# Kernel tuning notes

Hardware: AMD Instinct MI355X
Metric: run time of the kernel (lower is better)

## Reference

```python
import jax, jax.numpy as jnp
import numpy as np
import math

HIDDEN = 768
KEY = 128      # attention_key_size
INTER = 1536   # intermediate_size
B, S = 4, 2048


def setup_inputs() -> dict:
    key = jax.random.key(0)
    ks = jax.random.split(key, 8)
    hidden_states = jax.random.normal(ks[0], (B, S, HIDDEN), dtype=jnp.float32)
    attention_mask = jax.random.randint(ks[1], (B, 1, 1, S), 0, 2, dtype=jnp.int32)
    position_ids = jnp.arange(B * S, dtype=jnp.int32).reshape(B, S) % S
    Wi = jax.random.normal(ks[2], (HIDDEN, 2 * INTER + KEY), dtype=jnp.float32) * 0.02
    bi = jnp.zeros((2 * INTER + KEY,), dtype=jnp.float32)
    gamma = jax.random.normal(ks[3], (2, KEY), dtype=jnp.float32) * 0.02 + 1.0
    beta = jnp.zeros((2, KEY), dtype=jnp.float32)
    Wo = jax.random.normal(ks[4], (INTER, HIDDEN), dtype=jnp.float32) * 0.02
    bo = jnp.zeros((HIDDEN,), dtype=jnp.float32)
    return {"hidden_states": hidden_states, "attention_mask": attention_mask,
            "position_ids": position_ids, "Wi": Wi, "bi": bi,
            "gamma": gamma, "beta": beta, "Wo": Wo, "bo": bo}


def _gau_forward(hidden_states, attention_mask, Wi, bi, gamma, beta, Wo, bo):
    # i_dense + swish activation
    h = jax.nn.silu(jnp.einsum('bsd,de->bse', hidden_states, Wi) + bi)
    u = h[..., :INTER]
    v = h[..., INTER:2 * INTER]
    qk = h[..., 2 * INTER:]
    # OffsetScale: per-head affine (heads=2 -> q, k)
    q = qk * gamma[0] + beta[0]
    k = qk * gamma[1] + beta[1]
    scores = jnp.einsum('bid,bjd->bij', q, k) / math.sqrt(KEY)
    # additive mask: (1 - m) * -1e12, squeeze head dim
    am = (1.0 - attention_mask.astype(scores.dtype)) * -1e12
    scores = scores + am[:, 0]  # [B,1,S] broadcasts over query dim
    # softmax_plus normalization: scale logits by log(l)/log(512)
    valid = (scores > -1e11).astype(scores.dtype)
    l = jnp.maximum(jnp.sum(valid, axis=-1, keepdims=True), 1.0)
    scale = jnp.log(l) / jnp.log(jnp.asarray(512.0, scores.dtype))
    attn = jax.nn.softmax(scores * scale, axis=-1)
    ctx = jnp.einsum('bij,bjd->bid', attn, v)
    return jnp.einsum('bse,eh->bsh', u * ctx, Wo) + bo


def reference(hidden_states, attention_mask, position_ids, Wi, bi, gamma, beta, Wo, bo):
    # position_ids unused: p_bias is not 'rotary'
    return _gau_forward(hidden_states, attention_mask, Wi, bi, gamma, beta, Wo, bo)
```

## Files before the change

### kernel.cpp

```cpp
#include <hip/hip_runtime.h>
#include <math.h>

#define HIDDEN 768
#define KEY    128
#define INTER  1536
#define NB     4
#define SEQ    2048
#define MTOT   (NB*SEQ)
#define ETOT   (2*INTER+KEY)

typedef short bf16x8 __attribute__((ext_vector_type(8)));
typedef float f32x4  __attribute__((ext_vector_type(4)));

__device__ __forceinline__ unsigned short f2bfbits(float x) {
    union { float f; unsigned int u; } a; a.f = x;
    unsigned int r = a.u + 0x7fffu + ((a.u >> 16) & 1u);
    return (unsigned short)(r >> 16);
}
__device__ __forceinline__ float bfbits2f(unsigned short b) {
    union { float f; unsigned int u; } a; a.u = ((unsigned int)b) << 16;
    return a.f;
}

__device__ __forceinline__ void gl2lds16(const unsigned short* g, unsigned short* l) {
    __builtin_amdgcn_global_load_lds(
        (const __attribute__((address_space(1))) unsigned int*)g,
        (__attribute__((address_space(3))) unsigned int*)l, 16, 0, 0);
}

__global__ __launch_bounds__(256) void scale_kernel(const int* __restrict__ mask,
                                                    float* __restrict__ scaleb) {
    __shared__ int red[256];
    int b = blockIdx.x;
    int s = 0;
    for (int j = threadIdx.x; j < SEQ; j += 256)
        s += (mask[b*SEQ + j] != 0) ? 1 : 0;
    red[threadIdx.x] = s;
    __syncthreads();
    for (int step = 128; step > 0; step >>= 1) {
        if (threadIdx.x < step) red[threadIdx.x] += red[threadIdx.x + step];
        __syncthreads();
    }
    if (threadIdx.x == 0) {
        float l = fmaxf((float)red[0], 1.0f);
        scaleb[b] = logf(l) / logf(512.0f);
    }
}

__global__ __launch_bounds__(256) void cvt_bf16_kernel(const float* __restrict__ in,
                                                       unsigned short* __restrict__ out, int n4) {
    int i = blockIdx.x*256 + threadIdx.x;
    if (i < n4) {
        float4 v = ((const float4*)in)[i];
        ushort4 o;
        o.x = f2bfbits(v.x); o.y = f2bfbits(v.y);
        o.z = f2bfbits(v.z); o.w = f2bfbits(v.w);
        ((ushort4*)out)[i] = o;
    }
}

__global__ __launch_bounds__(256) void transpose_cvt(const float* __restrict__ in,
                                                     unsigned short* __restrict__ out,
                                                     int R, int C) {
    __shared__ unsigned short tile[32][33];
    int c0 = blockIdx.x*32, r0 = blockIdx.y*32;
    int tx = threadIdx.x & 31, ty4 = (threadIdx.x >> 5)*4;
    #pragma unroll
    for (int rr = 0; rr < 4; rr++) {
        int r = ty4 + rr;
        tile[r][tx] = f2bfbits(in[(size_t)(r0+r)*C + c0+tx]);
    }
    __syncthreads();
    #pragma unroll
    for (int rr = 0; rr < 4; rr++) {
        int r = ty4 + rr;
        out[(size_t)(c0+r)*R + r0+tx] = tile[tx][r];
    }
}

__global__ __launch_bounds__(256) void transpose_v(const unsigned short* __restrict__ v,
                                                   unsigned short* __restrict__ vT) {
    __shared__ unsigned short tile[32][33];
    int z = blockIdx.z;
    int c0 = blockIdx.x*32, s0 = blockIdx.y*32;
    int tx = threadIdx.x & 31, ty4 = (threadIdx.x >> 5)*4;
    #pragma unroll
    for (int rr = 0; rr < 4; rr++) {
        int s = ty4 + rr;
        tile[s][tx] = v[(size_t)(z*SEQ + s0+s)*INTER + c0+tx];
    }
    __syncthreads();
    #pragma unroll
    for (int rr = 0; rr < 4; rr++) {
        int c = ty4 + rr;
        vT[((size_t)z*INTER + c0+c)*SEQ + s0+tx] = tile[tx][c];
    }
}

__device__ __forceinline__ void mfma_core(
    const unsigned short* __restrict__ Abase, int lda,
    const unsigned short* __restrict__ Bbase, int ldb,
    unsigned short* As, unsigned short* Bs,
    f32x4 acc[4][4], int tid, int ktot)
{
    const int lane = tid & 63, wave = tid >> 6;
    const int wm = (wave >> 1) << 6, wn = (wave & 1) << 6;
    const int lm = lane & 15;
    const int q8 = (lane >> 4) << 3;
    const int row_a = tid >> 2, col_a = (tid & 3) << 3;
    const int row_b = row_a + 64;

    for (int k0 = 0; k0 < ktot; k0 += 32) {
        if (k0) __syncthreads();
        gl2lds16(Abase + (size_t)row_a*lda + k0 + col_a, As + tid*8);
        gl2lds16(Bbase + (size_t)row_a*ldb + k0 + col_a, Bs + tid*8);
        gl2lds16(Abase + (size_t)row_b*lda + k0 + col_a, As + (tid+256)*8);
        gl2lds16(Bbase + (size_t)row_b*ldb + k0 + col_a, Bs + (tid+256)*8);
        __syncthreads();
        bf16x8 af[4], bfr[4];
        #pragma unroll
        for (int i = 0; i < 4; i++)
            af[i] = *(const bf16x8*)&As[(wm + i*16 + lm)*32 + q8];
        #pragma unroll
        for (int j = 0; j < 4; j++)
            bfr[j] = *(const bf16x8*)&Bs[(wn + j*16 + lm)*32 + q8];
        #pragma unroll
        for (int i = 0; i < 4; i++)
            #pragma unroll
            for (int j = 0; j < 4; j++)
                acc[i][j] = __builtin_amdgcn_mfma_f32_16x16x32_bf16(af[i], bfr[j], acc[i][j], 0, 0, 0);
    }
}

#define EPILOG_IDX \
    const int lane = tid & 63, wave = tid >> 6; \
    const int wm = (wave >> 1) << 6, wn = (wave & 1) << 6; \
    const int cn = lane & 15, r4 = (lane >> 4) << 2;

__global__ __launch_bounds__(256) void gemm1_mfma(
    const unsigned short* __restrict__ Xb, const unsigned short* __restrict__ WiT,
    const float* __restrict__ bi, const float* __restrict__ gamma, const float* __restrict__ beta,
    unsigned short* __restrict__ u, unsigned short* __restrict__ v,
    unsigned short* __restrict__ qb, unsigned short* __restrict__ kb)
{
    __shared__ __align__(16) unsigned short As[128*32];
    __shared__ __align__(16) unsigned short Bs[128*32];
    const int tid = threadIdx.x;
    const int row0 = blockIdx.y*128, col0 = blockIdx.x*128;
    f32x4 acc[4][4];
    #pragma unroll
    for (int i = 0; i < 4; i++)
        #pragma unroll
        for (int j = 0; j < 4; j++)
            acc[i][j] = (f32x4){0.f,0.f,0.f,0.f};
    mfma_core(Xb + (size_t)row0*HIDDEN, HIDDEN, WiT + (size_t)col0*HIDDEN, HIDDEN,
              As, Bs, acc, tid, HIDDEN);
    EPILOG_IDX
    #pragma unroll
    for (int j = 0; j < 4; j++) {
        int n = col0 + wn + j*16 + cn;
        float bin = bi[n];
        #pragma unroll
        for (int i = 0; i < 4; i++) {
            #pragma unroll
            for (int r = 0; r < 4; r++) {
                int m = row0 + wm + i*16 + r4 + r;
                float x = acc[i][j][r] + bin;
                float h = x / (1.0f + __expf(-x));
                if (col0 < INTER) {
                    u[(size_t)m*INTER + n] = f2bfbits(h);
                } else if (col0 < 2*INTER) {
                    v[(size_t)m*INTER + (n - INTER)] = f2bfbits(h);
                } else {
                    int c = n - 2*INTER;
                    qb[(size_t)m*KEY + c] = f2bfbits(h*gamma[c]       + beta[c]);
                    kb[(size_t)m*KEY + c] = f2bfbits(h*gamma[KEY + c] + beta[KEY + c]);
                }
            }
        }
    }
}

__global__ __launch_bounds__(256) void attn_mfma(
    const unsigned short* __restrict__ qb, const unsigned short* __restrict__ kb,
    const int* __restrict__ mask, const float* __restrict__ scaleb,
    unsigned short* __restrict__ P)
{
    __shared__ __align__(16) unsigned short As[128*32];
    __shared__ __align__(16) unsigned short Bs[128*32];
    const int tid = threadIdx.x;
    const int z = blockIdx.z;
    const int row0 = blockIdx.y*128, col0 = blockIdx.x*128;
    f32x4 acc[4][4];
    #pragma unroll
    for (int i = 0; i < 4; i++)
        #pragma unroll
        for (int j = 0; j < 4; j++)
            acc[i][j] = (f32x4){0.f,0.f,0.f,0.f};
    mfma_core(qb + ((size_t)z*SEQ + row0)*KEY, KEY, kb + ((size_t)z*SEQ + col0)*KEY, KEY,
              As, Bs, acc, tid, KEY);
    const float st = scaleb[z] * 0.08838834764831845f;
    EPILOG_IDX
    #pragma unroll
    for (int j = 0; j < 4; j++) {
        int n = col0 + wn + j*16 + cn;
        int mk = mask[z*SEQ + n];
        #pragma unroll
        for (int i = 0; i < 4; i++) {
            #pragma unroll
            for (int r = 0; r < 4; r++) {
                int m = row0 + wm + i*16 + r4 + r;
                float p = mk ? __expf(acc[i][j][r]*st) : 0.0f;
                P[((size_t)z*SEQ + m)*SEQ + n] = f2bfbits(p);
            }
        }
    }
}

__global__ __launch_bounds__(256) void rowsum_kernel(const unsigned short* __restrict__ P,
                                                     float* __restrict__ lbuf) {
    int row = blockIdx.x*4 + (threadIdx.x >> 6);
    int lane = threadIdx.x & 63;
    const unsigned short* pr = P + (size_t)row*SEQ;
    float s = 0.f;
    for (int c = lane*8; c < SEQ; c += 64*8) {
        ushort4 a = *(const ushort4*)&pr[c];
        ushort4 b = *(const ushort4*)&pr[c+4];
        s += bfbits2f(a.x)+bfbits2f(a.y)+bfbits2f(a.z)+bfbits2f(a.w)
           + bfbits2f(b.x)+bfbits2f(b.y)+bfbits2f(b.z)+bfbits2f(b.w);
    }
    #pragma unroll
    for (int off = 32; off > 0; off >>= 1) s += __shfl_down(s, off, 64);
    if (lane == 0) lbuf[row] = s;
}

__global__ __launch_bounds__(256) void pv_mfma(
    const unsigned short* __restrict__ P, const unsigned short* __restrict__ vT,
    const float* __restrict__ lbuf, unsigned short* __restrict__ u)
{
    __shared__ __align__(16) unsigned short As[128*32];
    __shared__ __align__(16) unsigned short Bs[128*32];
    const int tid = threadIdx.x;
    const int z = blockIdx.z;
    const int row0 = blockIdx.y*128, col0 = blockIdx.x*128;
    f32x4 acc[4][4];
    #pragma unroll
    for (int i = 0; i < 4; i++)
        #pragma unroll
        for (int j = 0; j < 4; j++)
            acc[i][j] = (f32x4){0.f,0.f,0.f,0.f};
    mfma_core(P + ((size_t)z*SEQ + row0)*SEQ, SEQ, vT + ((size_t)z*INTER + col0)*SEQ, SEQ,
              As, Bs, acc, tid, SEQ);
    EPILOG_IDX
    #pragma unroll
    for (int i = 0; i < 4; i++) {
        #pragma unroll
        for (int r = 0; r < 4; r++) {
            int gm = z*SEQ + row0 + wm + i*16 + r4 + r;
            float linv = 1.0f / lbuf[gm];
            #pragma unroll
            for (int j = 0; j < 4; j++) {
                int n = col0 + wn + j*16 + cn;
                size_t idx = (size_t)gm*INTER + n;
                float uu = bfbits2f(u[idx]);
                u[idx] = f2bfbits(uu * acc[i][j][r] * linv);
            }
        }
    }
}

__global__ __launch_bounds__(256) void gemm2_mfma(
    const unsigned short* __restrict__ g, const unsigned short* __restrict__ WoT,
    const float* __restrict__ bo, float* __restrict__ out)
{
    __shared__ __align__(16) unsigned short As[128*32];
    __shared__ __align__(16) unsigned short Bs[128*32];
    const int tid = threadIdx.x;
    const int row0 = blockIdx.y*128, col0 = blockIdx.x*128;
    f32x4 acc[4][4];
    #pragma unroll
    for (int i = 0; i < 4; i++)
        #pragma unroll
        for (int j = 0; j < 4; j++)
            acc[i][j] = (f32x4){0.f,0.f,0.f,0.f};
    mfma_core(g + (size_t)row0*INTER, INTER, WoT + (size_t)col0*INTER, INTER,
              As, Bs, acc, tid, INTER);
    EPILOG_IDX
    #pragma unroll
    for (int j = 0; j < 4; j++) {
        int n = col0 + wn + j*16 + cn;
        float bon = bo[n];
        #pragma unroll
        for (int i = 0; i < 4; i++) {
            #pragma unroll
            for (int r = 0; r < 4; r++) {
                int m = row0 + wm + i*16 + r4 + r;
                out[(size_t)m*HIDDEN + n] = acc[i][j][r] + bon;
            }
        }
    }
}

extern "C" void kernel_launch(void* const* d_in, const int* in_sizes, int n_in,
                              void* d_out, int out_size, void* d_ws, size_t ws_size,
                              hipStream_t stream)
{
    const float* X     = (const float*)d_in[0];
    const int*   mask  = (const int*)d_in[1];
    const float* Wi    = (const float*)d_in[3];
    const float* bi    = (const float*)d_in[4];
    const float* gamma = (const float*)d_in[5];
    const float* beta  = (const float*)d_in[6];
    const float* Wo    = (const float*)d_in[7];
    const float* bo    = (const float*)d_in[8];
    float* out = (float*)d_out;

    unsigned short* Xb  = (unsigned short*)d_ws;
    unsigned short* WiT = Xb  + (size_t)MTOT*HIDDEN;
    unsigned short* WoT = WiT + (size_t)ETOT*HIDDEN;
    unsigned short* u   = WoT + (size_t)HIDDEN*INTER;
    unsigned short* v   = u   + (size_t)MTOT*INTER;
    unsigned short* vT  = v   + (size_t)MTOT*INTER;
    unsigned short* qb  = vT  + (size_t)MTOT*INTER;
    unsigned short* kb  = qb  + (size_t)MTOT*KEY;
    unsigned short* P   = kb  + (size_t)MTOT*KEY;
    float* lb  = (float*)(P + (size_t)NB*SEQ*SEQ);
    float* scb = lb + MTOT;

    scale_kernel<<<NB, 256, 0, stream>>>(mask, scb);
    cvt_bf16_kernel<<<(MTOT*HIDDEN/4 + 255)/256, 256, 0, stream>>>(X, Xb, MTOT*HIDDEN/4);
    transpose_cvt<<<dim3(ETOT/32, HIDDEN/32), 256, 0, stream>>>(Wi, WiT, HIDDEN, ETOT);
    transpose_cvt<<<dim3(HIDDEN/32, INTER/32), 256, 0, stream>>>(Wo, WoT, INTER, HIDDEN);
    gemm1_mfma<<<dim3(ETOT/128, MTOT/128), 256, 0, stream>>>(Xb, WiT, bi, gamma, beta, u, v, qb, kb);
    transpose_v<<<dim3(INTER/32, SEQ/32, NB), 256, 0, stream>>>(v, vT);
    attn_mfma<<<dim3(SEQ/128, SEQ/128, NB), 256, 0, stream>>>(qb, kb, mask, scb, P);
    rowsum_kernel<<<MTOT/4, 256, 0, stream>>>(P, lb);
    pv_mfma<<<dim3(INTER/128, SEQ/128, NB), 256, 0, stream>>>(P, vT, lb, u);
    gemm2_mfma<<<dim3(HIDDEN/128, MTOT/128), 256, 0, stream>>>(u, WoT, bo, out);
}
```

Before: 328.5 us.

## Stage GEMM epilogues through LDS for vectorized stores and fuse V transpose

The epilogues of gemm1, attn and pv now write their accumulator tiles into a padded shared-memory buffer, then emit 16-byte vectorized global stores instead of scattered 2-byte stores. gemm1 writes V directly in transposed layout from LDS, so the separate transpose_v kernel and the v buffer are gone. The pv epilogue now rounds the context to bf16 before multiplying by u, which adds a small extra rounding step. Shared memory per block grows to 128x136 shorts, which may reduce occupancy, and the extra barriers add some sync cost.

```diff
diff --git a/kernel.cpp b/kernel.cpp
--- a/kernel.cpp
+++ b/kernel.cpp
@@ -8,9 +8,11 @@
 #define SEQ    2048
 #define MTOT   (NB*SEQ)
 #define ETOT   (2*INTER+KEY)
+#define CS     136
 
 typedef short bf16x8 __attribute__((ext_vector_type(8)));
 typedef float f32x4  __attribute__((ext_vector_type(4)));
+typedef unsigned short u16x8 __attribute__((ext_vector_type(8)));
 
 __device__ __forceinline__ unsigned short f2bfbits(float x) {
     union { float f; unsigned int u; } a; a.f = x;
@@ -78,25 +80,6 @@
     }
 }
 
-__global__ __launch_bounds__(256) void transpose_v(const unsigned short* __restrict__ v,
-                                                   unsigned short* __restrict__ vT) {
-    __shared__ unsigned short tile[32][33];
-    int z = blockIdx.z;
-    int c0 = blockIdx.x*32, s0 = blockIdx.y*32;
-    int tx = threadIdx.x & 31, ty4 = (threadIdx.x >> 5)*4;
-    #pragma unroll
-    for (int rr = 0; rr < 4; rr++) {
-        int s = ty4 + rr;
-        tile[s][tx] = v[(size_t)(z*SEQ + s0+s)*INTER + c0+tx];
-    }
-    __syncthreads();
-    #pragma unroll
-    for (int rr = 0; rr < 4; rr++) {
-        int c = ty4 + rr;
-        vT[((size_t)z*INTER + c0+c)*SEQ + s0+tx] = tile[tx][c];
-    }
-}
-
 __device__ __forceinline__ void mfma_core(
     const unsigned short* __restrict__ Abase, int lda,
     const unsigned short* __restrict__ Bbase, int ldb,
@@ -140,11 +123,12 @@
 __global__ __launch_bounds__(256) void gemm1_mfma(
     const unsigned short* __restrict__ Xb, const unsigned short* __restrict__ WiT,
     const float* __restrict__ bi, const float* __restrict__ gamma, const float* __restrict__ beta,
-    unsigned short* __restrict__ u, unsigned short* __restrict__ v,
+    unsigned short* __restrict__ u, unsigned short* __restrict__ vT,
     unsigned short* __restrict__ qb, unsigned short* __restrict__ kb)
 {
-    __shared__ __align__(16) unsigned short As[128*32];
-    __shared__ __align__(16) unsigned short Bs[128*32];
+    __shared__ __align__(16) unsigned short smem[128*CS];
+    unsigned short* As = smem;
+    unsigned short* Bs = smem + 4096;
     const int tid = threadIdx.x;
     const int row0 = blockIdx.y*128, col0 = blockIdx.x*128;
     f32x4 acc[4][4];
@@ -156,27 +140,61 @@
     mfma_core(Xb + (size_t)row0*HIDDEN, HIDDEN, WiT + (size_t)col0*HIDDEN, HIDDEN,
               As, Bs, acc, tid, HIDDEN);
     EPILOG_IDX
+    __syncthreads();
     #pragma unroll
     for (int j = 0; j < 4; j++) {
-        int n = col0 + wn + j*16 + cn;
-        float bin = bi[n];
+        int nl = wn + j*16 + cn;
+        float bin = bi[col0 + nl];
         #pragma unroll
         for (int i = 0; i < 4; i++) {
             #pragma unroll
             for (int r = 0; r < 4; r++) {
-                int m = row0 + wm + i*16 + r4 + r;
+                int rowl = wm + i*16 + r4 + r;
                 float x = acc[i][j][r] + bin;
                 float h = x / (1.0f + __expf(-x));
-                if (col0 < INTER) {
-                    u[(size_t)m*INTER + n] = f2bfbits(h);
-                } else if (col0 < 2*INTER) {
-                    v[(size_t)m*INTER + (n - INTER)] = f2bfbits(h);
-                } else {
-                    int c = n - 2*INTER;
-                    qb[(size_t)m*KEY + c] = f2bfbits(h*gamma[c]       + beta[c]);
-                    kb[(size_t)m*KEY + c] = f2bfbits(h*gamma[KEY + c] + beta[KEY + c]);
-                }
-            }
+                smem[rowl*CS + nl] = f2bfbits(h);
+            }
+        }
+    }
+    __syncthreads();
+    if (col0 < INTER) {
+        #pragma unroll
+        for (int rnd = 0; rnd < 8; rnd++) {
+            int row = rnd*16 + (tid>>4);
+            int col = (tid&15)*8;
+            u16x8 h = *(const u16x8*)&smem[row*CS + col];
+            *(u16x8*)&u[(size_t)(row0+row)*INTER + col0 + col] = h;
+        }
+    } else if (col0 < 2*INTER) {
+        int c = tid >> 1;
+        int half = tid & 1;
+        int b = row0 / SEQ;
+        int srow = row0 - b*SEQ + half*64;
+        size_t base = ((size_t)b*INTER + (col0 - INTER) + c)*SEQ + srow;
+        #pragma unroll
+        for (int k = 0; k < 8; k++) {
+            u16x8 h;
+            #pragma unroll
+            for (int t = 0; t < 8; t++)
+                h[t] = smem[(half*64 + k*8 + t)*CS + c];
+            *(u16x8*)&vT[base + k*8] = h;
+        }
+    } else {
+        #pragma unroll
+        for (int rnd = 0; rnd < 8; rnd++) {
+            int row = rnd*16 + (tid>>4);
+            int col = (tid&15)*8;
+            u16x8 h = *(const u16x8*)&smem[row*CS + col];
+            int m = row0 + row;
+            u16x8 qo, ko;
+            #pragma unroll
+            for (int t = 0; t < 8; t++) {
+                float hv = bfbits2f(h[t]);
+                qo[t] = f2bfbits(hv*gamma[col+t]       + beta[col+t]);
+                ko[t] = f2bfbits(hv*gamma[KEY+col+t]   + beta[KEY+col+t]);
+            }
+            *(u16x8*)&qb[(size_t)m*KEY + col] = qo;
+            *(u16x8*)&kb[(size_t)m*KEY + col] = ko;
         }
     }
 }
@@ -186,8 +204,9 @@
     const int* __restrict__ mask, const float* __restrict__ scaleb,
     unsigned short* __restrict__ P)
 {
-    __shared__ __align__(16) unsigned short As[128*32];
-    __shared__ __align__(16) unsigned short Bs[128*32];
+    __shared__ __align__(16) unsigned short smem[128*CS];
+    unsigned short* As = smem;
+    unsigned short* Bs = smem + 4096;
     const int tid = threadIdx.x;
     const int z = blockIdx.z;
     const int row0 = blockIdx.y*128, col0 = blockIdx.x*128;
@@ -201,19 +220,28 @@
               As, Bs, acc, tid, KEY);
     const float st = scaleb[z] * 0.08838834764831845f;
     EPILOG_IDX
+    __syncthreads();
     #pragma unroll
     for (int j = 0; j < 4; j++) {
-        int n = col0 + wn + j*16 + cn;
-        int mk = mask[z*SEQ + n];
+        int nl = wn + j*16 + cn;
+        float mkf = (mask[z*SEQ + col0 + nl] != 0) ? 1.0f : 0.0f;
         #pragma unroll
         for (int i = 0; i < 4; i++) {
             #pragma unroll
             for (int r = 0; r < 4; r++) {
-                int m = row0 + wm + i*16 + r4 + r;
-                float p = mk ? __expf(acc[i][j][r]*st) : 0.0f;
-                P[((size_t)z*SEQ + m)*SEQ + n] = f2bfbits(p);
-            }
-        }
+                int rowl = wm + i*16 + r4 + r;
+                float p = mkf * __expf(acc[i][j][r]*st);
+                smem[rowl*CS + nl] = f2bfbits(p);
+            }
+        }
+    }
+    __syncthreads();
+    #pragma unroll
+    for (int rnd = 0; rnd < 8; rnd++) {
+        int row = rnd*16 + (tid>>4);
+        int col = (tid&15)*8;
+        u16x8 h = *(const u16x8*)&smem[row*CS + col];
+        *(u16x8*)&P[((size_t)z*SEQ + row0 + row)*SEQ + col0 + col] = h;
     }
 }
 
@@ -238,8 +266,9 @@
     const unsigned short* __restrict__ P, const unsigned short* __restrict__ vT,
     const float* __restrict__ lbuf, unsigned short* __restrict__ u)
 {
-    __shared__ __align__(16) unsigned short As[128*32];
-    __shared__ __align__(16) unsigned short Bs[128*32];
+    __shared__ __align__(16) unsigned short smem[128*CS];
+    unsigned short* As = smem;
+    unsigned short* Bs = smem + 4096;
     const int tid = threadIdx.x;
     const int z = blockIdx.z;
     const int row0 = blockIdx.y*128, col0 = blockIdx.x*128;
@@ -252,20 +281,34 @@
     mfma_core(P + ((size_t)z*SEQ + row0)*SEQ, SEQ, vT + ((size_t)z*INTER + col0)*SEQ, SEQ,
               As, Bs, acc, tid, SEQ);
     EPILOG_IDX
-    #pragma unroll
-    for (int i = 0; i < 4; i++) {
-        #pragma unroll
-        for (int r = 0; r < 4; r++) {
-            int gm = z*SEQ + row0 + wm + i*16 + r4 + r;
-            float linv = 1.0f / lbuf[gm];
-            #pragma unroll
-            for (int j = 0; j < 4; j++) {
-                int n = col0 + wn + j*16 + cn;
-                size_t idx = (size_t)gm*INTER + n;
-                float uu = bfbits2f(u[idx]);
-                u[idx] = f2bfbits(uu * acc[i][j][r] * linv);
-            }
-        }
+    __syncthreads();
+    #pragma unroll
+    for (int j = 0; j < 4; j++) {
+        int nl = wn + j*16 + cn;
+        #pragma unroll
+        for (int i = 0; i < 4; i++) {
+            #pragma unroll
+            for (int r = 0; r < 4; r++) {
+                int rowl = wm + i*16 + r4 + r;
+                smem[rowl*CS + nl] = f2bfbits(acc[i][j][r]);
+            }
+        }
+    }
+    __syncthreads();
+    #pragma unroll
+    for (int rnd = 0; rnd < 8; rnd++) {
+        int row = rnd*16 + (tid>>4);
+        int col = (tid&15)*8;
+        int m = z*SEQ + row0 + row;
+        float linv = 1.0f / lbuf[m];
+        u16x8 cx = *(const u16x8*)&smem[row*CS + col];
+        size_t idx = (size_t)m*INTER + col0 + col;
+        u16x8 uu = *(const u16x8*)&u[idx];
+        u16x8 g;
+        #pragma unroll
+        for (int t = 0; t < 8; t++)
+            g[t] = f2bfbits(bfbits2f(uu[t]) * bfbits2f(cx[t]) * linv);
+        *(u16x8*)&u[idx] = g;
     }
 }
 
@@ -319,8 +362,7 @@
     unsigned short* WiT = Xb  + (size_t)MTOT*HIDDEN;
     unsigned short* WoT = WiT + (size_t)ETOT*HIDDEN;
     unsigned short* u   = WoT + (size_t)HIDDEN*INTER;
-    unsigned short* v   = u   + (size_t)MTOT*INTER;
-    unsigned short* vT  = v   + (size_t)MTOT*INTER;
+    unsigned short* vT  = u   + (size_t)MTOT*INTER;
     unsigned short* qb  = vT  + (size_t)MTOT*INTER;
     unsigned short* kb  = qb  + (size_t)MTOT*KEY;
     unsigned short* P   = kb  + (size_t)MTOT*KEY;
@@ -331,8 +373,7 @@
     cvt_bf16_kernel<<<(MTOT*HIDDEN/4 + 255)/256, 256, 0, stream>>>(X, Xb, MTOT*HIDDEN/4);
     transpose_cvt<<<dim3(ETOT/32, HIDDEN/32), 256, 0, stream>>>(Wi, WiT, HIDDEN, ETOT);
     transpose_cvt<<<dim3(HIDDEN/32, INTER/32), 256, 0, stream>>>(Wo, WoT, INTER, HIDDEN);
-    gemm1_mfma<<<dim3(ETOT/128, MTOT/128), 256, 0, stream>>>(Xb, WiT, bi, gamma, beta, u, v, qb, kb);
-    transpose_v<<<dim3(INTER/32, SEQ/32, NB), 256, 0, stream>>>(v, vT);
+    gemm1_mfma<<<dim3(ETOT/128, MTOT/128), 256, 0, stream>>>(Xb, WiT, bi, gamma, beta, u, vT, qb, kb);
     attn_mfma<<<dim3(SEQ/128, SEQ/128, NB), 256, 0, stream>>>(qb, kb, mask, scb, P);
     rowsum_kernel<<<MTOT/4, 256, 0, stream>>>(P, lb);
     pv_mfma<<<dim3(INTER/128, SEQ/128, NB), 256, 0, stream>>>(P, vT, lb, u);
```

Result: faster. 318.3 us (-3.1%).
